# Optimization experiments

Measured on AMD Instinct MI355X. Metric: run time of the kernel, lower is better.

The kernel has to match this reference:

```python
import jax, jax.numpy as jnp
import numpy as np

EPS = 1e-12  # F.normalize default eps


def setup_inputs() -> dict:
    key = jax.random.key(0)
    ks = jax.random.split(key, 8)
    b, c, h, w = 8, 192, 128, 128
    s = 0.02
    return {
        "x_in": jax.random.normal(ks[0], (b, c, h, w), dtype=jnp.float32),
        "w_split": jax.random.normal(ks[1], (c, c), dtype=jnp.float32) * s,
        "w_q": jax.random.normal(ks[2], (c, c), dtype=jnp.float32) * s,
        "w_k": jax.random.normal(ks[3], (c, c), dtype=jnp.float32) * s,
        "w_v": jax.random.normal(ks[4], (c, c), dtype=jnp.float32) * s,
        "w_proj": jax.random.normal(ks[5], (c, c), dtype=jnp.float32) * s,
        "b_proj": jax.random.normal(ks[6], (c,), dtype=jnp.float32) * s,
        "w_out": jax.random.normal(ks[7], (c, c), dtype=jnp.float32) * s,
    }


def _l2norm(x):
    # F.normalize(p=2, dim=-1): x / max(||x||, eps)
    n = jnp.sqrt(jnp.sum(x * x, axis=-1, keepdims=True))
    return x / jnp.maximum(n, EPS)


def reference(x_in, w_split, w_q, w_k, w_v, w_proj, b_proj, w_out):
    b, c, h, w = x_in.shape
    # conv_split0: 1x1 conv, no bias -> channel matmul
    x = jnp.einsum('oc,bchw->bohw', w_split, x_in)
    # [b,h,w,c] -> [b,hw,c]
    x = x.transpose(0, 2, 3, 1).reshape(b, h * w, c)
    # Linear: y = x @ W^T
    q = jnp.einsum('bnc,oc->bon', x, w_q)  # [b,c,hw] (already transposed)
    k = jnp.einsum('bnc,oc->bon', x, w_k)
    v = jnp.einsum('bnc,oc->bon', x, w_v)
    q = _l2norm(q)
    k = _l2norm(k)
    attn = jax.nn.softmax(jnp.einsum('bcn,bdn->bcd', k, q), axis=-1)  # [b,c,c]
    y = jnp.einsum('bcd,bdn->bcn', attn, v)  # [b,c,hw]
    y = y.transpose(0, 2, 1)  # [b,hw,c]
    out = jnp.einsum('bnc,oc->bno', y, w_proj) + b_proj
    out = out.reshape(b, h, w, c).transpose(0, 3, 1, 2)  # [b,c,h,w]
    out = jnp.einsum('oc,bchw->bohw', w_out, out)
    return out
```

## Files before the change

kernel.cpp:

```cpp
#include <hip/hip_runtime.h>


static constexpr int B_ = 8;
static constexpr int C_ = 192;
static constexpr int N_ = 16384;
static constexpr int CC2 = C_ * C_;
static constexpr int NCHUNK = 32;

using u16x8 = __attribute__((ext_vector_type(8))) unsigned short;
using bf16x8 = __attribute__((ext_vector_type(8))) __bf16;
using f32x4 = __attribute__((ext_vector_type(4))) float;
using uint32x4 = __attribute__((ext_vector_type(4))) unsigned int;

__device__ __forceinline__ unsigned short f2bf(float f) {
  unsigned int u = __builtin_bit_cast(unsigned int, f);
  u += 0x7FFFu + ((u >> 16) & 1u);
  return (unsigned short)(u >> 16);
}

__device__ __forceinline__ unsigned int pkbf(float lo, float hi) {
  unsigned short a = __builtin_bit_cast(unsigned short, (__bf16)lo);
  unsigned short b = __builtin_bit_cast(unsigned short, (__bf16)hi);
  return (unsigned int)a | ((unsigned int)b << 16);
}

__device__ __forceinline__ u16x8 ld8bf(const float* p) {
  float4 u0 = *(const float4*)p;
  float4 u1 = *(const float4*)(p + 4);
  uint32x4 w;
  w[0] = pkbf(u0.x, u0.y); w[1] = pkbf(u0.z, u0.w);
  w[2] = pkbf(u1.x, u1.y); w[3] = pkbf(u1.z, u1.w);
  return __builtin_bit_cast(u16x8, w);
}

__device__ __forceinline__ float f4get(const float4& v, int e) {
  return (e == 0) ? v.x : (e == 1) ? v.y : (e == 2) ? v.z : v.w;
}

__device__ __forceinline__ f32x4 mfma16(u16x8 a, u16x8 b, f32x4 c) {
  return __builtin_amdgcn_mfma_f32_16x16x32_bf16(
      __builtin_bit_cast(bf16x8, a), __builtin_bit_cast(bf16x8, b), c, 0, 0, 0);
}

__device__ __forceinline__ void stage_f32_bf16(const float* __restrict__ src,
                                               unsigned short* __restrict__ lds,
                                               int tid) {
#pragma unroll
  for (int i = 0; i < 36; ++i) {
    int idx = i * 256 + tid;
    int row = idx / 48, c4 = idx % 48;
    float4 v = *(const float4*)(src + (size_t)row * C_ + c4 * 4);
    uint2 pk; pk.x = pkbf(v.x, v.y); pk.y = pkbf(v.z, v.w);
    *(uint2*)&lds[row * 200 + c4 * 4] = pk;
  }
}

__device__ __forceinline__ void stage_bf16(const unsigned short* __restrict__ src,
                                           unsigned short* __restrict__ lds, int tid) {
#pragma unroll
  for (int i = 0; i < 18; ++i) {
    int idx = i * 256 + tid;
    int row = idx / 24, c8 = idx % 24;
    uint4 v = *(const uint4*)(src + (size_t)row * C_ + c8 * 8);
    *(uint4*)&lds[row * 200 + c8 * 8] = v;
  }
}

__global__ void fold_kernel(const float* __restrict__ wsplit, const float* __restrict__ wq,
                            const float* __restrict__ wk, const float* __restrict__ wv,
                            const float* __restrict__ wproj, const float* __restrict__ bproj,
                            const float* __restrict__ wout,
                            float* __restrict__ Wq, float* __restrict__ WvT,
                            float* __restrict__ Wk, float* __restrict__ Wv,
                            float* __restrict__ Wo2, float* __restrict__ bias2) {
  int idx = blockIdx.x * 256 + threadIdx.x;
  if (idx < C_) {
    float s = 0.f;
    for (int c = 0; c < C_; ++c) s += wout[idx * C_ + c] * bproj[c];
    bias2[idx] = s;
  }
  if (idx >= 4 * CC2) return;
  int which = idx / CC2;
  int rem = idx % CC2;
  int o = rem / C_, c = rem % C_;
  const float* A = (which == 0) ? wq : (which == 1) ? wk : (which == 2) ? wv : wout;
  const float* Bm = (which == 3) ? wproj : wsplit;
  float s = 0.f;
  for (int e = 0; e < C_; ++e) s += A[o * C_ + e] * Bm[e * C_ + c];
  if (which == 0) Wq[rem] = s;
  else if (which == 1) Wk[rem] = s;
  else if (which == 2) { Wv[rem] = s; WvT[c * C_ + o] = s; }
  else Wo2[rem] = s;
}

template <bool ATOMIC>
__global__ __launch_bounds__(384) void gram3_kernel(const float* __restrict__ xin,
                                                    float* __restrict__ dst) {
  const int b = blockIdx.z, half = blockIdx.y, ch = blockIdx.x;
  const int k0 = ch * 512;
  __shared__ unsigned short Xs[2][C_][72];
  const int tid = threadIdx.x;
  const int wv = tid >> 6;
  const int lane = tid & 63;
  const int ln = lane & 15, mq = lane >> 4;
  const int arow0 = half * 96 + wv * 16;
  const int cbase = tid >> 4;
  const int k4 = tid & 15;
  const float* xb = xin + (size_t)b * C_ * N_;

  f32x4 acc[12];
#pragma unroll
  for (int j = 0; j < 12; ++j) acc[j] = (f32x4)0.0f;

  float4 ld[8];
  auto load_stage = [&](int kbase) {
#pragma unroll
    for (int j = 0; j < 8; ++j)
      ld[j] = *(const float4*)(xb + (size_t)(j * 24 + cbase) * N_ + kbase + k4 * 4);
  };
  auto write_stage = [&](int buf) {
#pragma unroll
    for (int j = 0; j < 8; ++j) {
      uint2 pk;
      pk.x = pkbf(ld[j].x, ld[j].y);
      pk.y = pkbf(ld[j].z, ld[j].w);
      *(uint2*)&Xs[buf][j * 24 + cbase][k4 * 4] = pk;
    }
  };

  load_stage(k0);
  write_stage(0);
  __syncthreads();
  for (int s = 0; s < 8; ++s) {
    if (s < 7) load_stage(k0 + (s + 1) * 64);
    const int cb = s & 1;
#pragma unroll
    for (int ks = 0; ks < 2; ++ks) {
      const int kk = ks * 32 + mq * 8;
      u16x8 a0 = *(const u16x8*)&Xs[cb][arow0 + ln][kk];
#pragma unroll
      for (int ct = 0; ct < 12; ++ct) {
        u16x8 bf = *(const u16x8*)&Xs[cb][ct * 16 + ln][kk];
        acc[ct] = mfma16(a0, bf, acc[ct]);
      }
    }
    if (s < 7) {
      write_stage(cb ^ 1);
      __syncthreads();
    }
  }
  float* out = ATOMIC ? dst + (size_t)b * CC2
                      : dst + ((size_t)b * NCHUNK + ch) * CC2;
#pragma unroll
  for (int ct = 0; ct < 12; ++ct)
#pragma unroll
    for (int r = 0; r < 4; ++r) {
      int row = arow0 + mq * 4 + r;
      int col = ct * 16 + ln;
      if (ATOMIC) atomicAdd(&out[row * C_ + col], acc[ct][r]);
      else out[row * C_ + col] = acc[ct][r];
    }
}

__global__ void gsum_kernel(const float* __restrict__ P, float* __restrict__ G) {
  const int j = (blockIdx.x * 256 + threadIdx.x) * 4;
  const int b = blockIdx.y;
  const float* base = P + (size_t)b * NCHUNK * CC2 + j;
  float4 s = {0.f, 0.f, 0.f, 0.f};
#pragma unroll
  for (int ch = 0; ch < NCHUNK; ++ch) {
    float4 v = *(const float4*)(base + (size_t)ch * CC2);
    s.x += v.x; s.y += v.y; s.z += v.z; s.w += v.w;
  }
  *(float4*)(G + (size_t)b * CC2 + j) = s;
}

__global__ __launch_bounds__(256, 2) void tkqn2_kernel(
    const float* __restrict__ Wk, const float* __restrict__ Wq,
    const float* __restrict__ G, float* __restrict__ Tk,
    float* __restrict__ kn, float* __restrict__ qn) {
  __shared__ __align__(16) unsigned short Gs[192 * 200];
  const int b = blockIdx.y;
  const int row0 = blockIdx.x * 64;
  const int tid = threadIdx.x;
  const int w = tid >> 6, lane = tid & 63;
  const int ln = lane & 15, mq = lane >> 4;
  const int rbase = row0 + w * 16;
  const bool isq = rbase >= C_;
  const float* W2 = isq ? Wq : Wk;
  const int rloc = isq ? rbase - C_ : rbase;
  const float* Gb = G + (size_t)b * CC2;

  u16x8 afr[6];
#pragma unroll
  for (int kc = 0; kc < 6; ++kc)
    afr[kc] = ld8bf(W2 + (size_t)(rloc + ln) * C_ + kc * 32 + mq * 8);

  stage_f32_bf16(Gb, Gs, tid);
  __syncthreads();

  f32x4 acc[12];
#pragma unroll
  for (int j = 0; j < 12; ++j) acc[j] = (f32x4)0.0f;
#pragma unroll
  for (int kc = 0; kc < 6; ++kc)
#pragma unroll
    for (int ct = 0; ct < 12; ++ct)
      acc[ct] = mfma16(afr[kc], *(const u16x8*)&Gs[(ct * 16 + ln) * 200 + kc * 32 + mq * 8],
                       acc[ct]);

  const float* wr = W2 + (size_t)(rloc + mq * 4) * C_;
  float nrm[4] = {0.f, 0.f, 0.f, 0.f};
#pragma unroll
  for (int ct = 0; ct < 12; ++ct)
#pragma unroll
    for (int r = 0; r < 4; ++r)
      nrm[r] += acc[ct][r] * wr[r * C_ + ct * 16 + ln];
#pragma unroll
  for (int m = 1; m < 16; m <<= 1)
#pragma unroll
    for (int r = 0; r < 4; ++r) nrm[r] += __shfl_xor(nrm[r], m);
  if (ln == 0) {
#pragma unroll
    for (int r = 0; r < 4; ++r) {
      float v = fmaxf(sqrtf(fmaxf(nrm[r], 0.f)), 1e-12f);
      int row = rbase + mq * 4 + r;
      if (row < C_) kn[b * 256 + row] = v;
      else qn[b * 256 + row - C_] = v;
    }
  }
  if (!isq) {
#pragma unroll
    for (int ct = 0; ct < 12; ++ct)
#pragma unroll
      for (int r = 0; r < 4; ++r)
        Tk[((size_t)b * C_ + rbase + mq * 4 + r) * C_ + ct * 16 + ln] = acc[ct][r];
  }
}

__global__ __launch_bounds__(256, 1) void attn2_kernel(
    const float* __restrict__ Tk, const float* __restrict__ Wq,
    const float* __restrict__ WvT, const float* __restrict__ kn,
    const float* __restrict__ qn, unsigned short* __restrict__ Tvt) {
  __shared__ __align__(16) unsigned short Ws[192 * 200];
  __shared__ __align__(16) unsigned short As[64 * 200];
  const int b = blockIdx.y;
  const int row0 = blockIdx.x * 64;
  const int tid = threadIdx.x;
  const int w = tid >> 6, lane = tid & 63;
  const int ln = lane & 15, mq = lane >> 4;
  const int rbase = row0 + w * 16;

  u16x8 afr[6];
#pragma unroll
  for (int kc = 0; kc < 6; ++kc)
    afr[kc] = ld8bf(Tk + ((size_t)b * C_ + rbase + ln) * C_ + kc * 32 + mq * 8);

  stage_f32_bf16(Wq, Ws, tid);
  __syncthreads();

  f32x4 acc[12];
#pragma unroll
  for (int j = 0; j < 12; ++j) acc[j] = (f32x4)0.0f;
#pragma unroll
  for (int kc = 0; kc < 6; ++kc)
#pragma unroll
    for (int ct = 0; ct < 12; ++ct)
      acc[ct] = mfma16(afr[kc], *(const u16x8*)&Ws[(ct * 16 + ln) * 200 + kc * 32 + mq * 8],
                       acc[ct]);

  float rkn[4], rqn[12];
#pragma unroll
  for (int r = 0; r < 4; ++r) rkn[r] = kn[b * 256 + rbase + mq * 4 + r];
#pragma unroll
  for (int ct = 0; ct < 12; ++ct) rqn[ct] = qn[b * 256 + ct * 16 + ln];

  float mx[4] = {-1e30f, -1e30f, -1e30f, -1e30f};
#pragma unroll
  for (int ct = 0; ct < 12; ++ct)
#pragma unroll
    for (int r = 0; r < 4; ++r) {
      float l = acc[ct][r] / (rkn[r] * rqn[ct]);
      acc[ct][r] = l;
      mx[r] = fmaxf(mx[r], l);
    }
#pragma unroll
  for (int m = 1; m < 16; m <<= 1)
#pragma unroll
    for (int r = 0; r < 4; ++r) mx[r] = fmaxf(mx[r], __shfl_xor(mx[r], m));
  float sm[4] = {0.f, 0.f, 0.f, 0.f};
#pragma unroll
  for (int ct = 0; ct < 12; ++ct)
#pragma unroll
    for (int r = 0; r < 4; ++r) {
      float e = expf(acc[ct][r] - mx[r]);
      acc[ct][r] = e;
      sm[r] += e;
    }
#pragma unroll
  for (int m = 1; m < 16; m <<= 1)
#pragma unroll
    for (int r = 0; r < 4; ++r) sm[r] += __shfl_xor(sm[r], m);
  float inv[4];
#pragma unroll
  for (int r = 0; r < 4; ++r) inv[r] = 1.f / sm[r];
#pragma unroll
  for (int ct = 0; ct < 12; ++ct)
#pragma unroll
    for (int r = 0; r < 4; ++r) {
      int lrow = w * 16 + mq * 4 + r;
      As[lrow * 200 + ct * 16 + ln] = f2bf(acc[ct][r] * inv[r]);
    }
  __syncthreads();

  stage_f32_bf16(WvT, Ws, tid);
  __syncthreads();

  f32x4 tv[12];
#pragma unroll
  for (int j = 0; j < 12; ++j) tv[j] = (f32x4)0.0f;
#pragma unroll
  for (int kc = 0; kc < 6; ++kc) {
    u16x8 a2 = *(const u16x8*)&As[(w * 16 + ln) * 200 + kc * 32 + mq * 8];
#pragma unroll
    for (int ct = 0; ct < 12; ++ct)
      tv[ct] = mfma16(a2, *(const u16x8*)&Ws[(ct * 16 + ln) * 200 + kc * 32 + mq * 8],
                      tv[ct]);
  }
#pragma unroll
  for (int ct = 0; ct < 12; ++ct) {
    uint2 pk;
    pk.x = pkbf(tv[ct][0], tv[ct][1]);
    pk.y = pkbf(tv[ct][2], tv[ct][3]);
    *(uint2*)&Tvt[((size_t)b * C_ + ct * 16 + ln) * C_ + row0 + w * 16 + mq * 4] = pk;
  }
}

__global__ __launch_bounds__(256, 2) void m2_kernel(
    const float* __restrict__ Wo2, const unsigned short* __restrict__ Tvt,
    float* __restrict__ Mw) {
  __shared__ __align__(16) unsigned short Ts2[192 * 200];
  const int b = blockIdx.y;
  const int row0 = blockIdx.x * 64;
  const int tid = threadIdx.x;
  const int w = tid >> 6, lane = tid & 63;
  const int ln = lane & 15, mq = lane >> 4;
  const int rbase = row0 + w * 16;

  u16x8 afr[6];
#pragma unroll
  for (int kc = 0; kc < 6; ++kc)
    afr[kc] = ld8bf(Wo2 + (size_t)(rbase + ln) * C_ + kc * 32 + mq * 8);

  stage_bf16(Tvt + (size_t)b * CC2, Ts2, tid);
  __syncthreads();

  f32x4 acc[12];
#pragma unroll
  for (int j = 0; j < 12; ++j) acc[j] = (f32x4)0.0f;
#pragma unroll
  for (int kc = 0; kc < 6; ++kc)
#pragma unroll
    for (int ct = 0; ct < 12; ++ct)
      acc[ct] = mfma16(afr[kc], *(const u16x8*)&Ts2[(ct * 16 + ln) * 200 + kc * 32 + mq * 8],
                       acc[ct]);
#pragma unroll
  for (int ct = 0; ct < 12; ++ct)
#pragma unroll
    for (int r = 0; r < 4; ++r)
      Mw[(size_t)b * CC2 + (rbase + mq * 4 + r) * C_ + ct * 16 + ln] = acc[ct][r];
}

__global__ __launch_bounds__(384, 4) void final3_kernel(const float* __restrict__ xin,
                                                        const float* __restrict__ Mw,
                                                        const float* __restrict__ bias2,
                                                        float* __restrict__ out) {
  const int b = blockIdx.y;
  const int p0 = blockIdx.x * 64;
  __shared__ __align__(16) unsigned short Ts[64 * 192];
  const int tid = threadIdx.x;
  const int wv = tid >> 6;
  const int lane = tid & 63;
  const int ln = lane & 15, mq = lane >> 4;
  const float* Mb = Mw + (size_t)b * CC2;

  const int c0 = (tid >> 3) * 4;
  const int pq = tid & 7;
  const float* xsrc = xin + ((size_t)b * C_ + c0) * N_ + p0 + pq * 4;

  float4 ldA[4], ldB[4];
#pragma unroll
  for (int l = 0; l < 4; ++l) ldA[l] = *(const float4*)(xsrc + (size_t)l * N_);

  u16x8 afr[6][2];
  float bo[2][4];
#pragma unroll
  for (int i = 0; i < 2; ++i) {
    int row = 32 * wv + 16 * i + ln;
#pragma unroll
    for (int kc = 0; kc < 6; ++kc)
      afr[kc][i] = ld8bf(Mb + row * C_ + kc * 32 + mq * 8);
#pragma unroll
    for (int r = 0; r < 4; ++r) bo[i][r] = bias2[32 * wv + 16 * i + mq * 4 + r];
  }

  auto stage_write = [&](const float4* ld, int sbase) {
#pragma unroll
    for (int e = 0; e < 4; ++e) {
      int p = sbase + pq * 4 + e;
      int idx = p * 192 + ((((c0 >> 3) ^ ((p >> 1) & 7)) << 3) | (c0 & 7));
      uint2 pk;
      pk.x = pkbf(f4get(ld[0], e), f4get(ld[1], e));
      pk.y = pkbf(f4get(ld[2], e), f4get(ld[3], e));
      *(uint2*)&Ts[idx] = pk;
    }
  };

  auto compute = [&](int pt) {
    const int p = pt * 16 + ln;
    const int pkey = (p >> 1) & 7;
    f32x4 acc0 = (f32x4)0.0f, acc1 = (f32x4)0.0f;
#pragma unroll
    for (int kc = 0; kc < 6; ++kc) {
      u16x8 bf = *(const u16x8*)&Ts[p * 192 + (((kc * 4 + mq) ^ pkey) << 3)];
      acc0 = mfma16(afr[kc][0], bf, acc0);
      acc1 = mfma16(afr[kc][1], bf, acc1);
    }
    const int pp = p0 + p;
#pragma unroll
    for (int r = 0; r < 4; ++r) {
      int row0 = 32 * wv + mq * 4 + r;
      out[((size_t)b * C_ + row0) * N_ + pp] = acc0[r] + bo[0][r];
      out[((size_t)b * C_ + row0 + 16) * N_ + pp] = acc1[r] + bo[1][r];
    }
  };

  stage_write(ldA, 0);
  __syncthreads();
#pragma unroll
  for (int l = 0; l < 4; ++l) ldB[l] = *(const float4*)(xsrc + 32 + (size_t)l * N_);
  compute(0);
  compute(1);
  stage_write(ldB, 32);
  __syncthreads();
  compute(2);
  compute(3);
}

extern "C" void kernel_launch(void* const* d_in, const int* in_sizes, int n_in,
                              void* d_out, int out_size, void* d_ws, size_t ws_size,
                              hipStream_t stream) {
  const float* xin    = (const float*)d_in[0];
  const float* wsplit = (const float*)d_in[1];
  const float* wq     = (const float*)d_in[2];
  const float* wk     = (const float*)d_in[3];
  const float* wv     = (const float*)d_in[4];
  const float* wproj  = (const float*)d_in[5];
  const float* bproj  = (const float*)d_in[6];
  const float* wout   = (const float*)d_in[7];
  float* out = (float*)d_out;

  float* ws = (float*)d_ws;
  float* G     = ws;
  float* Wq    = G + (size_t)B_ * CC2;
  float* WvT   = Wq + CC2;
  float* Wk    = WvT + CC2;
  float* Wv    = Wk + CC2;
  float* Wo2   = Wv + CC2;
  float* bias2 = Wo2 + CC2;
  float* Tk    = bias2 + 256;
  float* Tvt_f = Tk + (size_t)B_ * CC2;
  float* Mw    = Tvt_f + (size_t)B_ * CC2;
  float* qn    = Mw + (size_t)B_ * CC2;
  float* kn    = qn + 256 * B_;
  float* P     = kn + 256 * B_;

  size_t base_floats = (size_t)(P - ws);
  size_t need_bytes = (base_floats + (size_t)B_ * NCHUNK * CC2) * sizeof(float);
  bool use_partials = ws_size >= need_bytes;

  fold_kernel<<<(4 * CC2 + 255) / 256, 256, 0, stream>>>(
      wsplit, wq, wk, wv, wproj, bproj, wout, Wq, WvT, Wk, Wv, Wo2, bias2);
  if (use_partials) {
    gram3_kernel<false><<<dim3(NCHUNK, 2, B_), 384, 0, stream>>>(xin, P);
    gsum_kernel<<<dim3(CC2 / 1024, B_), 256, 0, stream>>>(P, G);
  } else {
    hipMemsetAsync(G, 0, (size_t)B_ * CC2 * sizeof(float), stream);
    gram3_kernel<true><<<dim3(NCHUNK, 2, B_), 384, 0, stream>>>(xin, G);
  }
  tkqn2_kernel<<<dim3(6, B_), 256, 0, stream>>>(Wk, Wq, G, Tk, kn, qn);
  attn2_kernel<<<dim3(3, B_), 256, 0, stream>>>(Tk, Wq, WvT, kn, qn,
                                                (unsigned short*)Tvt_f);
  m2_kernel<<<dim3(3, B_), 256, 0, stream>>>(Wo2, (const unsigned short*)Tvt_f, Mw);
  final3_kernel<<<dim3(N_ / 64, B_), 384, 0, stream>>>(xin, Mw, bias2, out);
}
```

Before: 312.3 us.

## Fuse Tk/norm, attention softmax and output-matrix kernels into one per-batch kernel

Replaces the three small-matrix kernels (Tk with k/q norms, attention softmax with value product, and output-weight product) with a single kernel that runs one 384-thread block per batch and keeps every intermediate in shared memory as bf16. This removes two kernel launches and the global-memory round trips for Tk, Tvt and the norm vectors. In exchange, only 8 blocks run the whole chain of dependent 192x192 GEMMs, so far fewer CUs are used and the work is serialized within each block.

```diff
diff --git a/kernel.cpp b/kernel.cpp
--- a/kernel.cpp
+++ b/kernel.cpp
@@ -40,30 +40,6 @@
 __device__ __forceinline__ f32x4 mfma16(u16x8 a, u16x8 b, f32x4 c) {
   return __builtin_amdgcn_mfma_f32_16x16x32_bf16(
       __builtin_bit_cast(bf16x8, a), __builtin_bit_cast(bf16x8, b), c, 0, 0, 0);
-}
-
-__device__ __forceinline__ void stage_f32_bf16(const float* __restrict__ src,
-                                               unsigned short* __restrict__ lds,
-                                               int tid) {
-#pragma unroll
-  for (int i = 0; i < 36; ++i) {
-    int idx = i * 256 + tid;
-    int row = idx / 48, c4 = idx % 48;
-    float4 v = *(const float4*)(src + (size_t)row * C_ + c4 * 4);
-    uint2 pk; pk.x = pkbf(v.x, v.y); pk.y = pkbf(v.z, v.w);
-    *(uint2*)&lds[row * 200 + c4 * 4] = pk;
-  }
-}
-
-__device__ __forceinline__ void stage_bf16(const unsigned short* __restrict__ src,
-                                           unsigned short* __restrict__ lds, int tid) {
-#pragma unroll
-  for (int i = 0; i < 18; ++i) {
-    int idx = i * 256 + tid;
-    int row = idx / 24, c8 = idx % 24;
-    uint4 v = *(const uint4*)(src + (size_t)row * C_ + c8 * 8);
-    *(uint4*)&lds[row * 200 + c8 * 8] = v;
-  }
 }
 
 __global__ void fold_kernel(const float* __restrict__ wsplit, const float* __restrict__ wq,
@@ -175,200 +151,225 @@
   *(float4*)(G + (size_t)b * CC2 + j) = s;
 }
 
-__global__ __launch_bounds__(256, 2) void tkqn2_kernel(
-    const float* __restrict__ Wk, const float* __restrict__ Wq,
-    const float* __restrict__ G, float* __restrict__ Tk,
-    float* __restrict__ kn, float* __restrict__ qn) {
-  __shared__ __align__(16) unsigned short Gs[192 * 200];
-  const int b = blockIdx.y;
-  const int row0 = blockIdx.x * 64;
+__global__ __launch_bounds__(384, 1) void middle8_kernel(
+    const float* __restrict__ G, const float* __restrict__ Wk,
+    const float* __restrict__ Wq, const float* __restrict__ WvT,
+    const float* __restrict__ Wo2, float* __restrict__ Mw) {
+  __shared__ __align__(16) unsigned short R1[192 * 200];
+  __shared__ __align__(16) unsigned short R2[192 * 200];
+  __shared__ float knl[C_], qnl[C_];
+  const int b = blockIdx.x;
   const int tid = threadIdx.x;
   const int w = tid >> 6, lane = tid & 63;
   const int ln = lane & 15, mq = lane >> 4;
-  const int rbase = row0 + w * 16;
-  const bool isq = rbase >= C_;
-  const float* W2 = isq ? Wq : Wk;
-  const int rloc = isq ? rbase - C_ : rbase;
-  const float* Gb = G + (size_t)b * CC2;
-
-  u16x8 afr[6];
-#pragma unroll
-  for (int kc = 0; kc < 6; ++kc)
-    afr[kc] = ld8bf(W2 + (size_t)(rloc + ln) * C_ + kc * 32 + mq * 8);
-
-  stage_f32_bf16(Gb, Gs, tid);
-  __syncthreads();
-
-  f32x4 acc[12];
-#pragma unroll
-  for (int j = 0; j < 12; ++j) acc[j] = (f32x4)0.0f;
-#pragma unroll
-  for (int kc = 0; kc < 6; ++kc)
+  const int r0 = w * 32;
+
+  auto stage = [&](const float* src, unsigned short* lds) {
+#pragma unroll
+    for (int i = 0; i < 24; ++i) {
+      int idx = i * 384 + tid;
+      int row = idx / 48, c4 = idx % 48;
+      float4 v = *(const float4*)(src + (size_t)row * C_ + c4 * 4);
+      uint2 pk; pk.x = pkbf(v.x, v.y); pk.y = pkbf(v.z, v.w);
+      *(uint2*)&lds[row * 200 + c4 * 4] = pk;
+    }
+  };
+
+  stage(G + (size_t)b * CC2, R1);
+  __syncthreads();
+
+  for (int pass = 0; pass < 2; ++pass) {
+    const float* W2 = pass ? Wq : Wk;
+    u16x8 afr[2][6];
+#pragma unroll
+    for (int i = 0; i < 2; ++i)
+#pragma unroll
+      for (int kc = 0; kc < 6; ++kc)
+        afr[i][kc] = ld8bf(W2 + (size_t)(r0 + i * 16 + ln) * C_ + kc * 32 + mq * 8);
+    f32x4 acc[2][12];
+#pragma unroll
+    for (int i = 0; i < 2; ++i)
+#pragma unroll
+      for (int j = 0; j < 12; ++j) acc[i][j] = (f32x4)0.0f;
+#pragma unroll
+    for (int kc = 0; kc < 6; ++kc)
+#pragma unroll
+      for (int ct = 0; ct < 12; ++ct) {
+        u16x8 g = *(const u16x8*)&R1[(ct * 16 + ln) * 200 + kc * 32 + mq * 8];
+        acc[0][ct] = mfma16(afr[0][kc], g, acc[0][ct]);
+        acc[1][ct] = mfma16(afr[1][kc], g, acc[1][ct]);
+      }
+#pragma unroll
+    for (int i = 0; i < 2; ++i) {
+      const float* wr = W2 + (size_t)(r0 + i * 16 + mq * 4) * C_;
+      float nrm[4] = {0.f, 0.f, 0.f, 0.f};
+#pragma unroll
+      for (int ct = 0; ct < 12; ++ct)
+#pragma unroll
+        for (int r = 0; r < 4; ++r)
+          nrm[r] += acc[i][ct][r] * wr[r * C_ + ct * 16 + ln];
+#pragma unroll
+      for (int m = 1; m < 16; m <<= 1)
+#pragma unroll
+        for (int r = 0; r < 4; ++r) nrm[r] += __shfl_xor(nrm[r], m);
+      if (ln == 0) {
+#pragma unroll
+        for (int r = 0; r < 4; ++r) {
+          float v = fmaxf(sqrtf(fmaxf(nrm[r], 0.f)), 1e-12f);
+          (pass ? qnl : knl)[r0 + i * 16 + mq * 4 + r] = v;
+        }
+      }
+    }
+    if (pass == 0) {
+#pragma unroll
+      for (int i = 0; i < 2; ++i)
+#pragma unroll
+        for (int ct = 0; ct < 12; ++ct)
+#pragma unroll
+          for (int r = 0; r < 4; ++r)
+            R2[(r0 + i * 16 + mq * 4 + r) * 200 + ct * 16 + ln] = f2bf(acc[i][ct][r]);
+    }
+  }
+  __syncthreads();
+  stage(Wq, R1);
+  __syncthreads();
+
+  f32x4 acc[2][12];
+  {
+    u16x8 afr[2][6];
+#pragma unroll
+    for (int i = 0; i < 2; ++i)
+#pragma unroll
+      for (int kc = 0; kc < 6; ++kc)
+        afr[i][kc] = *(const u16x8*)&R2[(r0 + i * 16 + ln) * 200 + kc * 32 + mq * 8];
+#pragma unroll
+    for (int i = 0; i < 2; ++i)
+#pragma unroll
+      for (int j = 0; j < 12; ++j) acc[i][j] = (f32x4)0.0f;
+#pragma unroll
+    for (int kc = 0; kc < 6; ++kc)
+#pragma unroll
+      for (int ct = 0; ct < 12; ++ct) {
+        u16x8 q = *(const u16x8*)&R1[(ct * 16 + ln) * 200 + kc * 32 + mq * 8];
+        acc[0][ct] = mfma16(afr[0][kc], q, acc[0][ct]);
+        acc[1][ct] = mfma16(afr[1][kc], q, acc[1][ct]);
+      }
+  }
+  float rqn[12];
+#pragma unroll
+  for (int ct = 0; ct < 12; ++ct) rqn[ct] = qnl[ct * 16 + ln];
+#pragma unroll
+  for (int i = 0; i < 2; ++i) {
+    float rkn[4];
+#pragma unroll
+    for (int r = 0; r < 4; ++r) rkn[r] = knl[r0 + i * 16 + mq * 4 + r];
+    float mx[4] = {-1e30f, -1e30f, -1e30f, -1e30f};
 #pragma unroll
     for (int ct = 0; ct < 12; ++ct)
-      acc[ct] = mfma16(afr[kc], *(const u16x8*)&Gs[(ct * 16 + ln) * 200 + kc * 32 + mq * 8],
-                       acc[ct]);
-
-  const float* wr = W2 + (size_t)(rloc + mq * 4) * C_;
-  float nrm[4] = {0.f, 0.f, 0.f, 0.f};
-#pragma unroll
-  for (int ct = 0; ct < 12; ++ct)
-#pragma unroll
-    for (int r = 0; r < 4; ++r)
-      nrm[r] += acc[ct][r] * wr[r * C_ + ct * 16 + ln];
-#pragma unroll
-  for (int m = 1; m < 16; m <<= 1)
-#pragma unroll
-    for (int r = 0; r < 4; ++r) nrm[r] += __shfl_xor(nrm[r], m);
-  if (ln == 0) {
-#pragma unroll
-    for (int r = 0; r < 4; ++r) {
-      float v = fmaxf(sqrtf(fmaxf(nrm[r], 0.f)), 1e-12f);
-      int row = rbase + mq * 4 + r;
-      if (row < C_) kn[b * 256 + row] = v;
-      else qn[b * 256 + row - C_] = v;
-    }
-  }
-  if (!isq) {
+#pragma unroll
+      for (int r = 0; r < 4; ++r) {
+        float l = acc[i][ct][r] / (rkn[r] * rqn[ct]);
+        acc[i][ct][r] = l;
+        mx[r] = fmaxf(mx[r], l);
+      }
+#pragma unroll
+    for (int m = 1; m < 16; m <<= 1)
+#pragma unroll
+      for (int r = 0; r < 4; ++r) mx[r] = fmaxf(mx[r], __shfl_xor(mx[r], m));
+    float sm[4] = {0.f, 0.f, 0.f, 0.f};
 #pragma unroll
     for (int ct = 0; ct < 12; ++ct)
 #pragma unroll
+      for (int r = 0; r < 4; ++r) {
+        float e = expf(acc[i][ct][r] - mx[r]);
+        acc[i][ct][r] = e;
+        sm[r] += e;
+      }
+#pragma unroll
+    for (int m = 1; m < 16; m <<= 1)
+#pragma unroll
+      for (int r = 0; r < 4; ++r) sm[r] += __shfl_xor(sm[r], m);
+    float inv[4];
+#pragma unroll
+    for (int r = 0; r < 4; ++r) inv[r] = 1.f / sm[r];
+#pragma unroll
+    for (int ct = 0; ct < 12; ++ct)
+#pragma unroll
+      for (int r = 0; r < 4; ++r) acc[i][ct][r] *= inv[r];
+  }
+  __syncthreads();
+#pragma unroll
+  for (int i = 0; i < 2; ++i)
+#pragma unroll
+    for (int ct = 0; ct < 12; ++ct)
+#pragma unroll
       for (int r = 0; r < 4; ++r)
-        Tk[((size_t)b * C_ + rbase + mq * 4 + r) * C_ + ct * 16 + ln] = acc[ct][r];
-  }
-}
-
-__global__ __launch_bounds__(256, 1) void attn2_kernel(
-    const float* __restrict__ Tk, const float* __restrict__ Wq,
-    const float* __restrict__ WvT, const float* __restrict__ kn,
-    const float* __restrict__ qn, unsigned short* __restrict__ Tvt) {
-  __shared__ __align__(16) unsigned short Ws[192 * 200];
-  __shared__ __align__(16) unsigned short As[64 * 200];
-  const int b = blockIdx.y;
-  const int row0 = blockIdx.x * 64;
-  const int tid = threadIdx.x;
-  const int w = tid >> 6, lane = tid & 63;
-  const int ln = lane & 15, mq = lane >> 4;
-  const int rbase = row0 + w * 16;
-
-  u16x8 afr[6];
-#pragma unroll
-  for (int kc = 0; kc < 6; ++kc)
-    afr[kc] = ld8bf(Tk + ((size_t)b * C_ + rbase + ln) * C_ + kc * 32 + mq * 8);
-
-  stage_f32_bf16(Wq, Ws, tid);
-  __syncthreads();
-
-  f32x4 acc[12];
-#pragma unroll
-  for (int j = 0; j < 12; ++j) acc[j] = (f32x4)0.0f;
-#pragma unroll
-  for (int kc = 0; kc < 6; ++kc)
-#pragma unroll
-    for (int ct = 0; ct < 12; ++ct)
-      acc[ct] = mfma16(afr[kc], *(const u16x8*)&Ws[(ct * 16 + ln) * 200 + kc * 32 + mq * 8],
-                       acc[ct]);
-
-  float rkn[4], rqn[12];
-#pragma unroll
-  for (int r = 0; r < 4; ++r) rkn[r] = kn[b * 256 + rbase + mq * 4 + r];
-#pragma unroll
-  for (int ct = 0; ct < 12; ++ct) rqn[ct] = qn[b * 256 + ct * 16 + ln];
-
-  float mx[4] = {-1e30f, -1e30f, -1e30f, -1e30f};
-#pragma unroll
-  for (int ct = 0; ct < 12; ++ct)
-#pragma unroll
-    for (int r = 0; r < 4; ++r) {
-      float l = acc[ct][r] / (rkn[r] * rqn[ct]);
-      acc[ct][r] = l;
-      mx[r] = fmaxf(mx[r], l);
-    }
-#pragma unroll
-  for (int m = 1; m < 16; m <<= 1)
-#pragma unroll
-    for (int r = 0; r < 4; ++r) mx[r] = fmaxf(mx[r], __shfl_xor(mx[r], m));
-  float sm[4] = {0.f, 0.f, 0.f, 0.f};
-#pragma unroll
-  for (int ct = 0; ct < 12; ++ct)
-#pragma unroll
-    for (int r = 0; r < 4; ++r) {
-      float e = expf(acc[ct][r] - mx[r]);
-      acc[ct][r] = e;
-      sm[r] += e;
-    }
-#pragma unroll
-  for (int m = 1; m < 16; m <<= 1)
-#pragma unroll
-    for (int r = 0; r < 4; ++r) sm[r] += __shfl_xor(sm[r], m);
-  float inv[4];
-#pragma unroll
-  for (int r = 0; r < 4; ++r) inv[r] = 1.f / sm[r];
-#pragma unroll
-  for (int ct = 0; ct < 12; ++ct)
-#pragma unroll
-    for (int r = 0; r < 4; ++r) {
-      int lrow = w * 16 + mq * 4 + r;
-      As[lrow * 200 + ct * 16 + ln] = f2bf(acc[ct][r] * inv[r]);
-    }
-  __syncthreads();
-
-  stage_f32_bf16(WvT, Ws, tid);
-  __syncthreads();
-
-  f32x4 tv[12];
-#pragma unroll
-  for (int j = 0; j < 12; ++j) tv[j] = (f32x4)0.0f;
-#pragma unroll
-  for (int kc = 0; kc < 6; ++kc) {
-    u16x8 a2 = *(const u16x8*)&As[(w * 16 + ln) * 200 + kc * 32 + mq * 8];
-#pragma unroll
-    for (int ct = 0; ct < 12; ++ct)
-      tv[ct] = mfma16(a2, *(const u16x8*)&Ws[(ct * 16 + ln) * 200 + kc * 32 + mq * 8],
-                      tv[ct]);
-  }
-#pragma unroll
-  for (int ct = 0; ct < 12; ++ct) {
-    uint2 pk;
-    pk.x = pkbf(tv[ct][0], tv[ct][1]);
-    pk.y = pkbf(tv[ct][2], tv[ct][3]);
-    *(uint2*)&Tvt[((size_t)b * C_ + ct * 16 + ln) * C_ + row0 + w * 16 + mq * 4] = pk;
-  }
-}
-
-__global__ __launch_bounds__(256, 2) void m2_kernel(
-    const float* __restrict__ Wo2, const unsigned short* __restrict__ Tvt,
-    float* __restrict__ Mw) {
-  __shared__ __align__(16) unsigned short Ts2[192 * 200];
-  const int b = blockIdx.y;
-  const int row0 = blockIdx.x * 64;
-  const int tid = threadIdx.x;
-  const int w = tid >> 6, lane = tid & 63;
-  const int ln = lane & 15, mq = lane >> 4;
-  const int rbase = row0 + w * 16;
-
-  u16x8 afr[6];
-#pragma unroll
-  for (int kc = 0; kc < 6; ++kc)
-    afr[kc] = ld8bf(Wo2 + (size_t)(rbase + ln) * C_ + kc * 32 + mq * 8);
-
-  stage_bf16(Tvt + (size_t)b * CC2, Ts2, tid);
-  __syncthreads();
-
-  f32x4 acc[12];
-#pragma unroll
-  for (int j = 0; j < 12; ++j) acc[j] = (f32x4)0.0f;
-#pragma unroll
-  for (int kc = 0; kc < 6; ++kc)
-#pragma unroll
-    for (int ct = 0; ct < 12; ++ct)
-      acc[ct] = mfma16(afr[kc], *(const u16x8*)&Ts2[(ct * 16 + ln) * 200 + kc * 32 + mq * 8],
-                       acc[ct]);
-#pragma unroll
-  for (int ct = 0; ct < 12; ++ct)
-#pragma unroll
-    for (int r = 0; r < 4; ++r)
-      Mw[(size_t)b * CC2 + (rbase + mq * 4 + r) * C_ + ct * 16 + ln] = acc[ct][r];
+        R2[(r0 + i * 16 + mq * 4 + r) * 200 + ct * 16 + ln] = f2bf(acc[i][ct][r]);
+  stage(WvT, R1);
+  __syncthreads();
+
+  f32x4 tv[2][12];
+  {
+    u16x8 afr[2][6];
+#pragma unroll
+    for (int i = 0; i < 2; ++i)
+#pragma unroll
+      for (int kc = 0; kc < 6; ++kc)
+        afr[i][kc] = *(const u16x8*)&R2[(r0 + i * 16 + ln) * 200 + kc * 32 + mq * 8];
+#pragma unroll
+    for (int i = 0; i < 2; ++i)
+#pragma unroll
+      for (int j = 0; j < 12; ++j) tv[i][j] = (f32x4)0.0f;
+#pragma unroll
+    for (int kc = 0; kc < 6; ++kc)
+#pragma unroll
+      for (int ct = 0; ct < 12; ++ct) {
+        u16x8 q = *(const u16x8*)&R1[(ct * 16 + ln) * 200 + kc * 32 + mq * 8];
+        tv[0][ct] = mfma16(afr[0][kc], q, tv[0][ct]);
+        tv[1][ct] = mfma16(afr[1][kc], q, tv[1][ct]);
+      }
+  }
+  __syncthreads();
+#pragma unroll
+  for (int i = 0; i < 2; ++i)
+#pragma unroll
+    for (int ct = 0; ct < 12; ++ct) {
+      uint2 pk;
+      pk.x = pkbf(tv[i][ct][0], tv[i][ct][1]);
+      pk.y = pkbf(tv[i][ct][2], tv[i][ct][3]);
+      *(uint2*)&R1[(ct * 16 + ln) * 200 + r0 + i * 16 + mq * 4] = pk;
+    }
+  __syncthreads();
+
+  {
+    u16x8 afr[2][6];
+#pragma unroll
+    for (int i = 0; i < 2; ++i)
+#pragma unroll
+      for (int kc = 0; kc < 6; ++kc)
+        afr[i][kc] = ld8bf(Wo2 + (size_t)(r0 + i * 16 + ln) * C_ + kc * 32 + mq * 8);
+    f32x4 mc[2][12];
+#pragma unroll
+    for (int i = 0; i < 2; ++i)
+#pragma unroll
+      for (int j = 0; j < 12; ++j) mc[i][j] = (f32x4)0.0f;
+#pragma unroll
+    for (int kc = 0; kc < 6; ++kc)
+#pragma unroll
+      for (int ct = 0; ct < 12; ++ct) {
+        u16x8 q = *(const u16x8*)&R1[(ct * 16 + ln) * 200 + kc * 32 + mq * 8];
+        mc[0][ct] = mfma16(afr[0][kc], q, mc[0][ct]);
+        mc[1][ct] = mfma16(afr[1][kc], q, mc[1][ct]);
+      }
+#pragma unroll
+    for (int i = 0; i < 2; ++i)
+#pragma unroll
+      for (int ct = 0; ct < 12; ++ct)
+#pragma unroll
+        for (int r = 0; r < 4; ++r)
+          Mw[(size_t)b * CC2 + (r0 + i * 16 + mq * 4 + r) * C_ + ct * 16 + ln] =
+              mc[i][ct][r];
+  }
 }
 
 __global__ __launch_bounds__(384, 4) void final3_kernel(const float* __restrict__ xin,
@@ -468,12 +469,8 @@
   float* Wv    = Wk + CC2;
   float* Wo2   = Wv + CC2;
   float* bias2 = Wo2 + CC2;
-  float* Tk    = bias2 + 256;
-  float* Tvt_f = Tk + (size_t)B_ * CC2;
-  float* Mw    = Tvt_f + (size_t)B_ * CC2;
-  float* qn    = Mw + (size_t)B_ * CC2;
-  float* kn    = qn + 256 * B_;
-  float* P     = kn + 256 * B_;
+  float* Mw    = bias2 + 256;
+  float* P     = Mw + (size_t)B_ * CC2;
 
   size_t base_floats = (size_t)(P - ws);
   size_t need_bytes = (base_floats + (size_t)B_ * NCHUNK * CC2) * sizeof(float);
@@ -488,9 +485,6 @@
     hipMemsetAsync(G, 0, (size_t)B_ * CC2 * sizeof(float), stream);
     gram3_kernel<true><<<dim3(NCHUNK, 2, B_), 384, 0, stream>>>(xin, G);
   }
-  tkqn2_kernel<<<dim3(6, B_), 256, 0, stream>>>(Wk, Wq, G, Tk, kn, qn);
-  attn2_kernel<<<dim3(3, B_), 256, 0, stream>>>(Tk, Wq, WvT, kn, qn,
-                                                (unsigned short*)Tvt_f);
-  m2_kernel<<<dim3(3, B_), 256, 0, stream>>>(Wo2, (const unsigned short*)Tvt_f, Mw);
+  middle8_kernel<<<dim3(B_), 384, 0, stream>>>(G, Wk, Wq, WvT, Wo2, Mw);
   final3_kernel<<<dim3(N_ / 64, B_), 384, 0, stream>>>(xin, Mw, bias2, out);
 }
```

Result: slower. 340.9 us (+9.1%).
